# Kernel optimization log

Hardware: AMD Instinct MI355X
Metric: run time of the kernel (lower is better)

## Reference

```python
import jax, jax.numpy as jnp
import numpy as np

B, P, F_IN, F_OUT = 4, 256, 512, 512
TAU = 0.07
EPS = 1e-05


def setup_inputs() -> dict:
    key = jax.random.key(0)
    k1, k2, k3 = jax.random.split(key, 3)
    inputs = jax.random.normal(k1, (B, P, F_IN), dtype=jnp.float32)
    labels = jax.random.normal(k2, (B, P, F_IN), dtype=jnp.float32)
    # xavier_uniform for fc.weight (out, in)
    limit = float(np.sqrt(6.0 / (F_IN + F_OUT)))
    W = jax.random.uniform(k3, (F_OUT, F_IN), dtype=jnp.float32, minval=-limit, maxval=limit)
    b = jnp.zeros((F_OUT,), dtype=jnp.float32)
    return {"inputs": inputs, "labels": labels, "W": W, "b": b}


def reference(inputs, labels, W, b):
    Bz, Pn, _ = labels.shape
    # pairwise L1 distance between label vectors: (B, P, P)
    d = jnp.sum(jnp.abs(labels[:, None, :, :] - labels[:, :, None, :]), axis=-1)
    idx = (d == 0).astype(jnp.float32)
    dist = idx / jnp.sum(idx, axis=-1, keepdims=True)  # (B, P, P) target distribution
    # fc + L2 normalize (torch F.normalize: divide by max(norm, 1e-12))
    h = jnp.einsum("bpf,of->bpo", inputs, W) + b
    nrm = jnp.sqrt(jnp.sum(h * h, axis=-1, keepdims=True))
    x = h / jnp.maximum(nrm, 1e-12)
    scores = jnp.einsum("bpd,bqd->bpq", x, x) / TAU
    probs = jnp.clip(jax.nn.softmax(scores, axis=-1), EPS, 1.0 - EPS)
    # kl_div(log(probs), dist, reduction='batchmean'): sum(dist*(log(dist)-log(probs))) / (B*P)
    log_probs = jnp.log(probs)
    pointwise = jnp.where(dist > 0, dist * (jnp.log(jnp.where(dist > 0, dist, 1.0)) - log_probs), 0.0)
    loss = jnp.sum(pointwise) / (Bz * Pn)
    return loss
```

## Files before the change

kernel.cpp:

```cpp
#include <hip/hip_runtime.h>


#define INV_TAU (1.0f / 0.07f)
#define EPSC 1e-5f

constexpr int Bz = 4;
constexpr int Pn = 256;
constexpr int Fdim = 512;
constexpr int Mrows = Bz * Pn;
constexpr size_t HP_STRIDE = (size_t)Mrows * Fdim;
constexpr size_t SP_STRIDE = (size_t)Bz * Pn * Pn;

__device__ __forceinline__ float wave_sum(float v) {
  #pragma unroll
  for (int o = 32; o > 0; o >>= 1) v += __shfl_down(v, o, 64);
  return v;
}
__device__ __forceinline__ float wave_max(float v) {
  #pragma unroll
  for (int o = 32; o > 0; o >>= 1) v = fmaxf(v, __shfl_down(v, o, 64));
  return v;
}
__device__ __forceinline__ unsigned long long mix64(unsigned long long z) {
  z ^= z >> 33; z *= 0xff51afd7ed558ccdULL;
  z ^= z >> 33; z *= 0xc4ceb9fe1a85ec53ULL;
  z ^= z >> 33; return z;
}

__global__ __launch_bounds__(512) void fc_sig(const float* __restrict__ A,
                                              const float* __restrict__ W,
                                              const float* __restrict__ labels,
                                              float* __restrict__ hp,
                                              ulonglong2* __restrict__ sig,
                                              float* __restrict__ acc,
                                              unsigned int* __restrict__ done) {
  const int t = threadIdx.x;
  const int bid = blockIdx.x + 16 * (blockIdx.y + 8 * blockIdx.z);
  if (bid == 0 && t == 0) { acc[0] = 0.0f; done[0] = 0u; }

  {
    const int g = t >> 6, lane = t & 63;
    if (g < 4) {
      const int row = bid * 4 + g;
      const uint4* l4 = (const uint4*)(labels + (size_t)row * Fdim);
      unsigned long long h1 = 0, h2 = 0;
      #pragma unroll
      for (int c = lane; c < Fdim / 4; c += 64) {
        uint4 w = l4[c];
        unsigned long long w01 = ((unsigned long long)w.y << 32) | w.x;
        unsigned long long w23 = ((unsigned long long)w.w << 32) | w.z;
        unsigned long long idx = (unsigned long long)c;
        h1 ^= mix64(w01 + idx * 0x9E3779B97F4A7C15ULL + 0x0123456789ABCDEFULL);
        h1 ^= mix64(w23 + idx * 0xC2B2AE3D27D4EB4FULL + 1ULL);
        h2 ^= mix64(w01 ^ (idx * 0x165667B19E3779F9ULL + 7ULL));
        h2 ^= mix64(w23 ^ (idx * 0x27D4EB2F165667C5ULL + 13ULL));
      }
      #pragma unroll
      for (int o = 32; o > 0; o >>= 1) {
        h1 ^= __shfl_down(h1, o, 64);
        h2 ^= __shfl_down(h2, o, 64);
      }
      if (lane == 0) { sig[row].x = h1; sig[row].y = h2; }
    }
  }

  const int m0 = blockIdx.x * 64, n0 = blockIdx.y * 64;
  const int kbase = blockIdx.z * 256;
  float* C = hp + (size_t)blockIdx.z * HP_STRIDE;
  __shared__ float Ash[32][68];
  __shared__ float Bsh[32][68];
  const int tx = t & 15, ty = t >> 4;
  const int r0 = t >> 3, c0 = (t & 7) << 2;
  float acc2[2][4] = {};

  for (int kc = 0; kc < 256; kc += 32) {
    const float* Ap = A + (size_t)(m0 + r0) * Fdim + kbase + kc + c0;
    const float* Wp = W + (size_t)(n0 + r0) * Fdim + kbase + kc + c0;
    float4 a = *(const float4*)Ap;
    float4 b = *(const float4*)Wp;
    __syncthreads();
    Ash[c0+0][r0] = a.x; Ash[c0+1][r0] = a.y; Ash[c0+2][r0] = a.z; Ash[c0+3][r0] = a.w;
    Bsh[c0+0][r0] = b.x; Bsh[c0+1][r0] = b.y; Bsh[c0+2][r0] = b.z; Bsh[c0+3][r0] = b.w;
    __syncthreads();
    #pragma unroll 8
    for (int k = 0; k < 32; ++k) {
      float2 av = *(const float2*)&Ash[k][ty << 1];
      float4 bv = *(const float4*)&Bsh[k][tx << 2];
      acc2[0][0] = fmaf(av.x, bv.x, acc2[0][0]); acc2[0][1] = fmaf(av.x, bv.y, acc2[0][1]);
      acc2[0][2] = fmaf(av.x, bv.z, acc2[0][2]); acc2[0][3] = fmaf(av.x, bv.w, acc2[0][3]);
      acc2[1][0] = fmaf(av.y, bv.x, acc2[1][0]); acc2[1][1] = fmaf(av.y, bv.y, acc2[1][1]);
      acc2[1][2] = fmaf(av.y, bv.z, acc2[1][2]); acc2[1][3] = fmaf(av.y, bv.w, acc2[1][3]);
    }
  }
  #pragma unroll
  for (int i = 0; i < 2; ++i) {
    float4 o; o.x = acc2[i][0]; o.y = acc2[i][1]; o.z = acc2[i][2]; o.w = acc2[i][3];
    *(float4*)(C + (size_t)(m0 + (ty << 1) + i) * Fdim + n0 + (tx << 2)) = o;
  }
}

__global__ __launch_bounds__(512) void score_gemm(const float* __restrict__ hp,
                                                  const float* __restrict__ bias,
                                                  float* __restrict__ Sp) {
  const int b = blockIdx.z >> 2, kz = blockIdx.z & 3;
  const int kbase = kz * 128;
  const int m0 = blockIdx.x * 64, n0 = blockIdx.y * 64;
  const float* h0 = hp;
  const float* h1 = hp + HP_STRIDE;
  float* C = Sp + (size_t)kz * SP_STRIDE + (size_t)b * Pn * Pn;
  const size_t rb = (size_t)b * Pn;
  __shared__ float Ash[32][68];
  __shared__ float Bsh[32][68];
  const int t = threadIdx.x, tx = t & 15, ty = t >> 4;
  const int r0 = t >> 3, c0 = (t & 7) << 2;
  float acc2[2][4] = {};

  for (int kc = 0; kc < 128; kc += 32) {
    const int ko = kbase + kc + c0;
    float4 bi = *(const float4*)(bias + ko);
    size_t aoff = (rb + m0 + r0) * Fdim + ko;
    size_t boff = (rb + n0 + r0) * Fdim + ko;
    float4 al = *(const float4*)(h0 + aoff);
    float4 ah = *(const float4*)(h1 + aoff);
    float4 bl = *(const float4*)(h0 + boff);
    float4 bh = *(const float4*)(h1 + boff);
    float4 a, b;
    a.x = al.x + ah.x + bi.x; a.y = al.y + ah.y + bi.y;
    a.z = al.z + ah.z + bi.z; a.w = al.w + ah.w + bi.w;
    b.x = bl.x + bh.x + bi.x; b.y = bl.y + bh.y + bi.y;
    b.z = bl.z + bh.z + bi.z; b.w = bl.w + bh.w + bi.w;
    __syncthreads();
    Ash[c0+0][r0] = a.x; Ash[c0+1][r0] = a.y; Ash[c0+2][r0] = a.z; Ash[c0+3][r0] = a.w;
    Bsh[c0+0][r0] = b.x; Bsh[c0+1][r0] = b.y; Bsh[c0+2][r0] = b.z; Bsh[c0+3][r0] = b.w;
    __syncthreads();
    #pragma unroll 8
    for (int k = 0; k < 32; ++k) {
      float2 av = *(const float2*)&Ash[k][ty << 1];
      float4 bv = *(const float4*)&Bsh[k][tx << 2];
      acc2[0][0] = fmaf(av.x, bv.x, acc2[0][0]); acc2[0][1] = fmaf(av.x, bv.y, acc2[0][1]);
      acc2[0][2] = fmaf(av.x, bv.z, acc2[0][2]); acc2[0][3] = fmaf(av.x, bv.w, acc2[0][3]);
      acc2[1][0] = fmaf(av.y, bv.x, acc2[1][0]); acc2[1][1] = fmaf(av.y, bv.y, acc2[1][1]);
      acc2[1][2] = fmaf(av.y, bv.z, acc2[1][2]); acc2[1][3] = fmaf(av.y, bv.w, acc2[1][3]);
    }
  }
  #pragma unroll
  for (int i = 0; i < 2; ++i) {
    float4 o; o.x = acc2[i][0]; o.y = acc2[i][1]; o.z = acc2[i][2]; o.w = acc2[i][3];
    *(float4*)(C + (size_t)(m0 + (ty << 1) + i) * Pn + n0 + (tx << 2)) = o;
  }
}

__global__ __launch_bounds__(256) void loss_kernel(const float* __restrict__ Sp,
                                                   const ulonglong2* __restrict__ sig,
                                                   const float* __restrict__ labels,
                                                   float* __restrict__ acc,
                                                   unsigned int* __restrict__ done,
                                                   float* __restrict__ out) {
  const int bx = blockIdx.x;
  const int b = bx >> 6, p0 = (bx & 63) * 4;
  const int q = threadIdx.x;
  __shared__ float invn[256];
  __shared__ float red[12];
  const float* S0 = Sp + (size_t)b * Pn * Pn;
  const float* S1 = S0 + SP_STRIDE;
  const float* S2 = S0 + 2 * SP_STRIDE;
  const float* S3 = S0 + 3 * SP_STRIDE;

  {
    const int d = q * 257;
    float Sqq = S0[d] + S1[d] + S2[d] + S3[d];
    invn[q] = 1.0f / fmaxf(sqrtf(Sqq), 1e-12f);
  }
  const ulonglong2 sq = sig[(b << 8) + q];
  __syncthreads();

  const int w = q >> 6;
  float lane_contrib = 0.0f;

  #pragma unroll
  for (int i = 0; i < 4; ++i) {
    const int p = p0 + i;
    const int ro = p << 8;
    float Spq = S0[ro + q] + S1[ro + q] + S2[ro + q] + S3[ro + q];
    float s = Spq * invn[p] * invn[q] * INV_TAU;

    ulonglong2 sp = sig[(b << 8) + p];
    bool eq;
    if (q == p) eq = true;
    else if (sp.x == sq.x && sp.y == sq.y) {
      bool v = true;
      const float* lp = labels + (size_t)((b << 8) + p) * Fdim;
      const float* lq = labels + (size_t)((b << 8) + q) * Fdim;
      for (int j = 0; j < Fdim; ++j) v = v && (lp[j] == lq[j]);
      eq = v;
    } else eq = false;

    float m = wave_max(s);
    if ((q & 63) == 0) red[w] = m;
    __syncthreads();
    m = fmaxf(fmaxf(red[0], red[1]), fmaxf(red[2], red[3]));

    float e = expf(s - m);
    float zc = wave_sum(e);
    float cc = wave_sum(eq ? 1.0f : 0.0f);
    if ((q & 63) == 0) { red[4 + w] = zc; red[8 + w] = cc; }
    __syncthreads();
    float z = red[4] + red[5] + red[6] + red[7];
    float n = red[8] + red[9] + red[10] + red[11];

    float prob = fminf(fmaxf(e / z, EPSC), 1.0f - EPSC);
    if (eq) lane_contrib += (-logf(n) - logf(prob)) / n;
    __syncthreads();
  }

  float c = wave_sum(lane_contrib);
  if ((q & 63) == 0) red[w] = c;
  __syncthreads();
  if (q == 0) {
    atomicAdd(acc, red[0] + red[1] + red[2] + red[3]);
    __threadfence();
    unsigned int v = atomicAdd(done, 1u);
    if (v == 255u) {
      float tot = atomicAdd(acc, 0.0f);
      out[0] = tot * (1.0f / (float)(Bz * Pn));
    }
  }
}

extern "C" void kernel_launch(void* const* d_in, const int* in_sizes, int n_in,
                              void* d_out, int out_size, void* d_ws, size_t ws_size,
                              hipStream_t stream) {
  const float* inputs = (const float*)d_in[0];
  const float* labels = (const float*)d_in[1];
  const float* W      = (const float*)d_in[2];
  const float* bias   = (const float*)d_in[3];
  float* out = (float*)d_out;

  char* ws = (char*)d_ws;
  float* acc         = (float*)ws;
  unsigned int* done = (unsigned int*)(ws + 4);
  float* hp = (float*)(ws + 256);
  float* Sp = (float*)(ws + 256 + 2 * HP_STRIDE * 4);
  ulonglong2* sig = (ulonglong2*)(ws + 256 + 2 * HP_STRIDE * 4 + 4 * SP_STRIDE * 4);

  fc_sig<<<dim3(16, 8, 2), 512, 0, stream>>>(inputs, W, labels, hp, sig, acc, done);
  score_gemm<<<dim3(4, 4, 16), 512, 0, stream>>>(hp, bias, Sp);
  loss_kernel<<<256, 256, 0, stream>>>(Sp, sig, labels, acc, done, out);
}
```

Measured before the change: 99.07 us.

## Double-buffer GEMM tiles, 4x4 microtiles, fold bias, restructure loss softmax per wave

Both GEMM kernels now run 256 threads, each computing a 4x4 register microtile, and prefetch the next K-slice into registers while computing on a double-buffered shared-memory tile. This drops one barrier per iteration and overlaps global loads with FMAs. The bias is added once in the first FC split instead of on every score-GEMM load, and the score GEMM writes the diagonal norms to a small buffer. The loss kernel assigns one row per wave with four columns per lane, removing block-level barriers from the softmax reductions. The trade-offs are fewer threads per block and higher register pressure.

```diff
diff --git a/kernel.cpp b/kernel.cpp
--- a/kernel.cpp
+++ b/kernel.cpp
@@ -13,12 +13,12 @@
 
 __device__ __forceinline__ float wave_sum(float v) {
   #pragma unroll
-  for (int o = 32; o > 0; o >>= 1) v += __shfl_down(v, o, 64);
+  for (int o = 32; o > 0; o >>= 1) v += __shfl_xor(v, o, 64);
   return v;
 }
 __device__ __forceinline__ float wave_max(float v) {
   #pragma unroll
-  for (int o = 32; o > 0; o >>= 1) v = fmaxf(v, __shfl_down(v, o, 64));
+  for (int o = 32; o > 0; o >>= 1) v = fmaxf(v, __shfl_xor(v, o, 64));
   return v;
 }
 __device__ __forceinline__ unsigned long long mix64(unsigned long long z) {
@@ -27,8 +27,9 @@
   z ^= z >> 33; return z;
 }
 
-__global__ __launch_bounds__(512) void fc_sig(const float* __restrict__ A,
+__global__ __launch_bounds__(256) void fc_sig(const float* __restrict__ A,
                                               const float* __restrict__ W,
+                                              const float* __restrict__ bias,
                                               const float* __restrict__ labels,
                                               float* __restrict__ hp,
                                               ulonglong2* __restrict__ sig,
@@ -40,68 +41,100 @@
 
   {
     const int g = t >> 6, lane = t & 63;
-    if (g < 4) {
-      const int row = bid * 4 + g;
-      const uint4* l4 = (const uint4*)(labels + (size_t)row * Fdim);
-      unsigned long long h1 = 0, h2 = 0;
-      #pragma unroll
-      for (int c = lane; c < Fdim / 4; c += 64) {
-        uint4 w = l4[c];
-        unsigned long long w01 = ((unsigned long long)w.y << 32) | w.x;
-        unsigned long long w23 = ((unsigned long long)w.w << 32) | w.z;
-        unsigned long long idx = (unsigned long long)c;
-        h1 ^= mix64(w01 + idx * 0x9E3779B97F4A7C15ULL + 0x0123456789ABCDEFULL);
-        h1 ^= mix64(w23 + idx * 0xC2B2AE3D27D4EB4FULL + 1ULL);
-        h2 ^= mix64(w01 ^ (idx * 0x165667B19E3779F9ULL + 7ULL));
-        h2 ^= mix64(w23 ^ (idx * 0x27D4EB2F165667C5ULL + 13ULL));
-      }
-      #pragma unroll
-      for (int o = 32; o > 0; o >>= 1) {
-        h1 ^= __shfl_down(h1, o, 64);
-        h2 ^= __shfl_down(h2, o, 64);
-      }
-      if (lane == 0) { sig[row].x = h1; sig[row].y = h2; }
-    }
+    const int row = bid * 4 + g;
+    const uint4* l4 = (const uint4*)(labels + (size_t)row * Fdim);
+    unsigned long long h1 = 0, h2 = 0;
+    #pragma unroll
+    for (int c = lane; c < Fdim / 4; c += 64) {
+      uint4 wv = l4[c];
+      unsigned long long w01 = ((unsigned long long)wv.y << 32) | wv.x;
+      unsigned long long w23 = ((unsigned long long)wv.w << 32) | wv.z;
+      unsigned long long idx = (unsigned long long)c;
+      h1 ^= mix64(w01 + idx * 0x9E3779B97F4A7C15ULL + 0x0123456789ABCDEFULL);
+      h1 ^= mix64(w23 + idx * 0xC2B2AE3D27D4EB4FULL + 1ULL);
+      h2 ^= mix64(w01 ^ (idx * 0x165667B19E3779F9ULL + 7ULL));
+      h2 ^= mix64(w23 ^ (idx * 0x27D4EB2F165667C5ULL + 13ULL));
+    }
+    #pragma unroll
+    for (int o = 32; o > 0; o >>= 1) {
+      h1 ^= __shfl_down(h1, o, 64);
+      h2 ^= __shfl_down(h2, o, 64);
+    }
+    if (lane == 0) { sig[row].x = h1; sig[row].y = h2; }
   }
 
   const int m0 = blockIdx.x * 64, n0 = blockIdx.y * 64;
   const int kbase = blockIdx.z * 256;
   float* C = hp + (size_t)blockIdx.z * HP_STRIDE;
-  __shared__ float Ash[32][68];
-  __shared__ float Bsh[32][68];
+  __shared__ float Ash[2][32][68];
+  __shared__ float Bsh[2][32][68];
   const int tx = t & 15, ty = t >> 4;
-  const int r0 = t >> 3, c0 = (t & 7) << 2;
-  float acc2[2][4] = {};
-
+  const int sr = t >> 3, sc = (t & 7) << 2;
+
+  const float* Abase = A + (size_t)(m0 + sr) * Fdim + kbase + sc;
+  const float* Wbase = W + (size_t)(n0 + sr) * Fdim + kbase + sc;
+  float4 ra0, ra1, rb0, rb1;
+
+  auto store_tile = [&](int buf) {
+    Ash[buf][sc+0][sr] = ra0.x; Ash[buf][sc+1][sr] = ra0.y;
+    Ash[buf][sc+2][sr] = ra0.z; Ash[buf][sc+3][sr] = ra0.w;
+    Ash[buf][sc+0][sr+32] = ra1.x; Ash[buf][sc+1][sr+32] = ra1.y;
+    Ash[buf][sc+2][sr+32] = ra1.z; Ash[buf][sc+3][sr+32] = ra1.w;
+    Bsh[buf][sc+0][sr] = rb0.x; Bsh[buf][sc+1][sr] = rb0.y;
+    Bsh[buf][sc+2][sr] = rb0.z; Bsh[buf][sc+3][sr] = rb0.w;
+    Bsh[buf][sc+0][sr+32] = rb1.x; Bsh[buf][sc+1][sr+32] = rb1.y;
+    Bsh[buf][sc+2][sr+32] = rb1.z; Bsh[buf][sc+3][sr+32] = rb1.w;
+  };
+
+  ra0 = *(const float4*)(Abase);
+  ra1 = *(const float4*)(Abase + 32 * Fdim);
+  rb0 = *(const float4*)(Wbase);
+  rb1 = *(const float4*)(Wbase + 32 * Fdim);
+  store_tile(0);
+  __syncthreads();
+
+  float acc4[4][4] = {};
+
+  #pragma unroll
   for (int kc = 0; kc < 256; kc += 32) {
-    const float* Ap = A + (size_t)(m0 + r0) * Fdim + kbase + kc + c0;
-    const float* Wp = W + (size_t)(n0 + r0) * Fdim + kbase + kc + c0;
-    float4 a = *(const float4*)Ap;
-    float4 b = *(const float4*)Wp;
-    __syncthreads();
-    Ash[c0+0][r0] = a.x; Ash[c0+1][r0] = a.y; Ash[c0+2][r0] = a.z; Ash[c0+3][r0] = a.w;
-    Bsh[c0+0][r0] = b.x; Bsh[c0+1][r0] = b.y; Bsh[c0+2][r0] = b.z; Bsh[c0+3][r0] = b.w;
-    __syncthreads();
+    const int cur = (kc >> 5) & 1;
+    if (kc + 32 < 256) {
+      ra0 = *(const float4*)(Abase + kc + 32);
+      ra1 = *(const float4*)(Abase + kc + 32 + 32 * Fdim);
+      rb0 = *(const float4*)(Wbase + kc + 32);
+      rb1 = *(const float4*)(Wbase + kc + 32 + 32 * Fdim);
+    }
     #pragma unroll 8
     for (int k = 0; k < 32; ++k) {
-      float2 av = *(const float2*)&Ash[k][ty << 1];
-      float4 bv = *(const float4*)&Bsh[k][tx << 2];
-      acc2[0][0] = fmaf(av.x, bv.x, acc2[0][0]); acc2[0][1] = fmaf(av.x, bv.y, acc2[0][1]);
-      acc2[0][2] = fmaf(av.x, bv.z, acc2[0][2]); acc2[0][3] = fmaf(av.x, bv.w, acc2[0][3]);
-      acc2[1][0] = fmaf(av.y, bv.x, acc2[1][0]); acc2[1][1] = fmaf(av.y, bv.y, acc2[1][1]);
-      acc2[1][2] = fmaf(av.y, bv.z, acc2[1][2]); acc2[1][3] = fmaf(av.y, bv.w, acc2[1][3]);
-    }
-  }
-  #pragma unroll
-  for (int i = 0; i < 2; ++i) {
-    float4 o; o.x = acc2[i][0]; o.y = acc2[i][1]; o.z = acc2[i][2]; o.w = acc2[i][3];
-    *(float4*)(C + (size_t)(m0 + (ty << 1) + i) * Fdim + n0 + (tx << 2)) = o;
-  }
-}
-
-__global__ __launch_bounds__(512) void score_gemm(const float* __restrict__ hp,
-                                                  const float* __restrict__ bias,
-                                                  float* __restrict__ Sp) {
+      float4 av = *(const float4*)&Ash[cur][k][ty << 2];
+      float4 bv = *(const float4*)&Bsh[cur][k][tx << 2];
+      acc4[0][0] = fmaf(av.x, bv.x, acc4[0][0]); acc4[0][1] = fmaf(av.x, bv.y, acc4[0][1]);
+      acc4[0][2] = fmaf(av.x, bv.z, acc4[0][2]); acc4[0][3] = fmaf(av.x, bv.w, acc4[0][3]);
+      acc4[1][0] = fmaf(av.y, bv.x, acc4[1][0]); acc4[1][1] = fmaf(av.y, bv.y, acc4[1][1]);
+      acc4[1][2] = fmaf(av.y, bv.z, acc4[1][2]); acc4[1][3] = fmaf(av.y, bv.w, acc4[1][3]);
+      acc4[2][0] = fmaf(av.z, bv.x, acc4[2][0]); acc4[2][1] = fmaf(av.z, bv.y, acc4[2][1]);
+      acc4[2][2] = fmaf(av.z, bv.z, acc4[2][2]); acc4[2][3] = fmaf(av.z, bv.w, acc4[2][3]);
+      acc4[3][0] = fmaf(av.w, bv.x, acc4[3][0]); acc4[3][1] = fmaf(av.w, bv.y, acc4[3][1]);
+      acc4[3][2] = fmaf(av.w, bv.z, acc4[3][2]); acc4[3][3] = fmaf(av.w, bv.w, acc4[3][3]);
+    }
+    if (kc + 32 < 256) store_tile(cur ^ 1);
+    __syncthreads();
+  }
+
+  float4 bi = make_float4(0.0f, 0.0f, 0.0f, 0.0f);
+  if (blockIdx.z == 0) bi = *(const float4*)(bias + n0 + (tx << 2));
+  #pragma unroll
+  for (int i = 0; i < 4; ++i) {
+    float4 o;
+    o.x = acc4[i][0] + bi.x; o.y = acc4[i][1] + bi.y;
+    o.z = acc4[i][2] + bi.z; o.w = acc4[i][3] + bi.w;
+    *(float4*)(C + (size_t)(m0 + (ty << 2) + i) * Fdim + n0 + (tx << 2)) = o;
+  }
+}
+
+__global__ __launch_bounds__(256) void score_gemm(const float* __restrict__ hp,
+                                                  float* __restrict__ Sp,
+                                                  float* __restrict__ dn) {
   const int b = blockIdx.z >> 2, kz = blockIdx.z & 3;
   const int kbase = kz * 128;
   const int m0 = blockIdx.x * 64, n0 = blockIdx.y * 64;
@@ -109,112 +142,155 @@
   const float* h1 = hp + HP_STRIDE;
   float* C = Sp + (size_t)kz * SP_STRIDE + (size_t)b * Pn * Pn;
   const size_t rb = (size_t)b * Pn;
-  __shared__ float Ash[32][68];
-  __shared__ float Bsh[32][68];
+  __shared__ float Ash[2][32][68];
+  __shared__ float Bsh[2][32][68];
   const int t = threadIdx.x, tx = t & 15, ty = t >> 4;
-  const int r0 = t >> 3, c0 = (t & 7) << 2;
-  float acc2[2][4] = {};
-
+  const int sr = t >> 3, sc = (t & 7) << 2;
+  const size_t aoff = (rb + m0 + sr) * Fdim + kbase + sc;
+  const size_t boff = (rb + n0 + sr) * Fdim + kbase + sc;
+
+  float4 la0, ha0, la1, ha1, lb0, hb0, lb1, hb1;
+
+  auto load_tile = [&](int kc) {
+    la0 = *(const float4*)(h0 + aoff + kc);
+    ha0 = *(const float4*)(h1 + aoff + kc);
+    la1 = *(const float4*)(h0 + aoff + kc + 32 * Fdim);
+    ha1 = *(const float4*)(h1 + aoff + kc + 32 * Fdim);
+    lb0 = *(const float4*)(h0 + boff + kc);
+    hb0 = *(const float4*)(h1 + boff + kc);
+    lb1 = *(const float4*)(h0 + boff + kc + 32 * Fdim);
+    hb1 = *(const float4*)(h1 + boff + kc + 32 * Fdim);
+  };
+  auto store_tile = [&](int buf) {
+    float4 a0, a1, b0v, b1v;
+    a0.x = la0.x + ha0.x; a0.y = la0.y + ha0.y; a0.z = la0.z + ha0.z; a0.w = la0.w + ha0.w;
+    a1.x = la1.x + ha1.x; a1.y = la1.y + ha1.y; a1.z = la1.z + ha1.z; a1.w = la1.w + ha1.w;
+    b0v.x = lb0.x + hb0.x; b0v.y = lb0.y + hb0.y; b0v.z = lb0.z + hb0.z; b0v.w = lb0.w + hb0.w;
+    b1v.x = lb1.x + hb1.x; b1v.y = lb1.y + hb1.y; b1v.z = lb1.z + hb1.z; b1v.w = lb1.w + hb1.w;
+    Ash[buf][sc+0][sr] = a0.x; Ash[buf][sc+1][sr] = a0.y;
+    Ash[buf][sc+2][sr] = a0.z; Ash[buf][sc+3][sr] = a0.w;
+    Ash[buf][sc+0][sr+32] = a1.x; Ash[buf][sc+1][sr+32] = a1.y;
+    Ash[buf][sc+2][sr+32] = a1.z; Ash[buf][sc+3][sr+32] = a1.w;
+    Bsh[buf][sc+0][sr] = b0v.x; Bsh[buf][sc+1][sr] = b0v.y;
+    Bsh[buf][sc+2][sr] = b0v.z; Bsh[buf][sc+3][sr] = b0v.w;
+    Bsh[buf][sc+0][sr+32] = b1v.x; Bsh[buf][sc+1][sr+32] = b1v.y;
+    Bsh[buf][sc+2][sr+32] = b1v.z; Bsh[buf][sc+3][sr+32] = b1v.w;
+  };
+
+  load_tile(0);
+  store_tile(0);
+  __syncthreads();
+
+  float acc4[4][4] = {};
+
+  #pragma unroll
   for (int kc = 0; kc < 128; kc += 32) {
-    const int ko = kbase + kc + c0;
-    float4 bi = *(const float4*)(bias + ko);
-    size_t aoff = (rb + m0 + r0) * Fdim + ko;
-    size_t boff = (rb + n0 + r0) * Fdim + ko;
-    float4 al = *(const float4*)(h0 + aoff);
-    float4 ah = *(const float4*)(h1 + aoff);
-    float4 bl = *(const float4*)(h0 + boff);
-    float4 bh = *(const float4*)(h1 + boff);
-    float4 a, b;
-    a.x = al.x + ah.x + bi.x; a.y = al.y + ah.y + bi.y;
-    a.z = al.z + ah.z + bi.z; a.w = al.w + ah.w + bi.w;
-    b.x = bl.x + bh.x + bi.x; b.y = bl.y + bh.y + bi.y;
-    b.z = bl.z + bh.z + bi.z; b.w = bl.w + bh.w + bi.w;
-    __syncthreads();
-    Ash[c0+0][r0] = a.x; Ash[c0+1][r0] = a.y; Ash[c0+2][r0] = a.z; Ash[c0+3][r0] = a.w;
-    Bsh[c0+0][r0] = b.x; Bsh[c0+1][r0] = b.y; Bsh[c0+2][r0] = b.z; Bsh[c0+3][r0] = b.w;
-    __syncthreads();
+    const int cur = (kc >> 5) & 1;
+    if (kc + 32 < 128) load_tile(kc + 32);
     #pragma unroll 8
     for (int k = 0; k < 32; ++k) {
-      float2 av = *(const float2*)&Ash[k][ty << 1];
-      float4 bv = *(const float4*)&Bsh[k][tx << 2];
-      acc2[0][0] = fmaf(av.x, bv.x, acc2[0][0]); acc2[0][1] = fmaf(av.x, bv.y, acc2[0][1]);
-      acc2[0][2] = fmaf(av.x, bv.z, acc2[0][2]); acc2[0][3] = fmaf(av.x, bv.w, acc2[0][3]);
-      acc2[1][0] = fmaf(av.y, bv.x, acc2[1][0]); acc2[1][1] = fmaf(av.y, bv.y, acc2[1][1]);
-      acc2[1][2] = fmaf(av.y, bv.z, acc2[1][2]); acc2[1][3] = fmaf(av.y, bv.w, acc2[1][3]);
-    }
-  }
-  #pragma unroll
-  for (int i = 0; i < 2; ++i) {
-    float4 o; o.x = acc2[i][0]; o.y = acc2[i][1]; o.z = acc2[i][2]; o.w = acc2[i][3];
-    *(float4*)(C + (size_t)(m0 + (ty << 1) + i) * Pn + n0 + (tx << 2)) = o;
+      float4 av = *(const float4*)&Ash[cur][k][ty << 2];
+      float4 bv = *(const float4*)&Bsh[cur][k][tx << 2];
+      acc4[0][0] = fmaf(av.x, bv.x, acc4[0][0]); acc4[0][1] = fmaf(av.x, bv.y, acc4[0][1]);
+      acc4[0][2] = fmaf(av.x, bv.z, acc4[0][2]); acc4[0][3] = fmaf(av.x, bv.w, acc4[0][3]);
+      acc4[1][0] = fmaf(av.y, bv.x, acc4[1][0]); acc4[1][1] = fmaf(av.y, bv.y, acc4[1][1]);
+      acc4[1][2] = fmaf(av.y, bv.z, acc4[1][2]); acc4[1][3] = fmaf(av.y, bv.w, acc4[1][3]);
+      acc4[2][0] = fmaf(av.z, bv.x, acc4[2][0]); acc4[2][1] = fmaf(av.z, bv.y, acc4[2][1]);
+      acc4[2][2] = fmaf(av.z, bv.z, acc4[2][2]); acc4[2][3] = fmaf(av.z, bv.w, acc4[2][3]);
+      acc4[3][0] = fmaf(av.w, bv.x, acc4[3][0]); acc4[3][1] = fmaf(av.w, bv.y, acc4[3][1]);
+      acc4[3][2] = fmaf(av.w, bv.z, acc4[3][2]); acc4[3][3] = fmaf(av.w, bv.w, acc4[3][3]);
+    }
+    if (kc + 32 < 128) store_tile(cur ^ 1);
+    __syncthreads();
+  }
+
+  #pragma unroll
+  for (int i = 0; i < 4; ++i) {
+    float4 o; o.x = acc4[i][0]; o.y = acc4[i][1]; o.z = acc4[i][2]; o.w = acc4[i][3];
+    *(float4*)(C + (size_t)(m0 + (ty << 2) + i) * Pn + n0 + (tx << 2)) = o;
+  }
+  if (m0 == n0 && tx == ty) {
+    #pragma unroll
+    for (int i = 0; i < 4; ++i)
+      dn[(size_t)kz * Mrows + rb + m0 + (ty << 2) + i] = acc4[i][i];
   }
 }
 
 __global__ __launch_bounds__(256) void loss_kernel(const float* __restrict__ Sp,
                                                    const ulonglong2* __restrict__ sig,
                                                    const float* __restrict__ labels,
+                                                   const float* __restrict__ dn,
                                                    float* __restrict__ acc,
                                                    unsigned int* __restrict__ done,
                                                    float* __restrict__ out) {
   const int bx = blockIdx.x;
   const int b = bx >> 6, p0 = (bx & 63) * 4;
   const int q = threadIdx.x;
+  const int w = q >> 6, lane = q & 63;
   __shared__ float invn[256];
-  __shared__ float red[12];
+  __shared__ float red[4];
   const float* S0 = Sp + (size_t)b * Pn * Pn;
   const float* S1 = S0 + SP_STRIDE;
   const float* S2 = S0 + 2 * SP_STRIDE;
   const float* S3 = S0 + 3 * SP_STRIDE;
 
   {
-    const int d = q * 257;
-    float Sqq = S0[d] + S1[d] + S2[d] + S3[d];
-    invn[q] = 1.0f / fmaxf(sqrtf(Sqq), 1e-12f);
-  }
-  const ulonglong2 sq = sig[(b << 8) + q];
+    const int iq = (b << 8) + q;
+    float d = dn[iq] + dn[Mrows + iq] + dn[2 * Mrows + iq] + dn[3 * Mrows + iq];
+    invn[q] = 1.0f / fmaxf(sqrtf(d), 1e-12f);
+  }
   __syncthreads();
 
-  const int w = q >> 6;
-  float lane_contrib = 0.0f;
-
-  #pragma unroll
-  for (int i = 0; i < 4; ++i) {
-    const int p = p0 + i;
-    const int ro = p << 8;
-    float Spq = S0[ro + q] + S1[ro + q] + S2[ro + q] + S3[ro + q];
-    float s = Spq * invn[p] * invn[q] * INV_TAU;
-
-    ulonglong2 sp = sig[(b << 8) + p];
+  const int p = p0 + w;
+  const int ro = p << 8;
+  const ulonglong2 sp = sig[(b << 8) + p];
+  const float ip = invn[p];
+
+  float s[4];
+  unsigned eqm = 0;
+  #pragma unroll
+  for (int c = 0; c < 4; ++c) {
+    const int qq = (c << 6) + lane;
+    float Sv = S0[ro + qq] + S1[ro + qq] + S2[ro + qq] + S3[ro + qq];
+    s[c] = Sv * ip * invn[qq] * INV_TAU;
     bool eq;
-    if (q == p) eq = true;
-    else if (sp.x == sq.x && sp.y == sq.y) {
-      bool v = true;
-      const float* lp = labels + (size_t)((b << 8) + p) * Fdim;
-      const float* lq = labels + (size_t)((b << 8) + q) * Fdim;
-      for (int j = 0; j < Fdim; ++j) v = v && (lp[j] == lq[j]);
-      eq = v;
-    } else eq = false;
-
-    float m = wave_max(s);
-    if ((q & 63) == 0) red[w] = m;
-    __syncthreads();
-    m = fmaxf(fmaxf(red[0], red[1]), fmaxf(red[2], red[3]));
-
-    float e = expf(s - m);
-    float zc = wave_sum(e);
-    float cc = wave_sum(eq ? 1.0f : 0.0f);
-    if ((q & 63) == 0) { red[4 + w] = zc; red[8 + w] = cc; }
-    __syncthreads();
-    float z = red[4] + red[5] + red[6] + red[7];
-    float n = red[8] + red[9] + red[10] + red[11];
-
-    float prob = fminf(fmaxf(e / z, EPSC), 1.0f - EPSC);
-    if (eq) lane_contrib += (-logf(n) - logf(prob)) / n;
-    __syncthreads();
-  }
-
-  float c = wave_sum(lane_contrib);
-  if ((q & 63) == 0) red[w] = c;
+    if (qq == p) eq = true;
+    else {
+      ulonglong2 sq = sig[(b << 8) + qq];
+      if (sq.x == sp.x && sq.y == sp.y) {
+        bool v = true;
+        const float* lp = labels + (size_t)((b << 8) + p) * Fdim;
+        const float* lq = labels + (size_t)((b << 8) + qq) * Fdim;
+        for (int j = 0; j < Fdim; ++j) v = v && (lp[j] == lq[j]);
+        eq = v;
+      } else eq = false;
+    }
+    if (eq) eqm |= (1u << c);
+  }
+
+  float m = fmaxf(fmaxf(s[0], s[1]), fmaxf(s[2], s[3]));
+  m = wave_max(m);
+
+  float e[4], z = 0.0f, n = 0.0f;
+  #pragma unroll
+  for (int c = 0; c < 4; ++c) {
+    e[c] = expf(s[c] - m);
+    z += e[c];
+    n += ((eqm >> c) & 1u) ? 1.0f : 0.0f;
+  }
+  z = wave_sum(z);
+  n = wave_sum(n);
+
+  float contrib = 0.0f;
+  #pragma unroll
+  for (int c = 0; c < 4; ++c) {
+    if ((eqm >> c) & 1u) {
+      float prob = fminf(fmaxf(e[c] / z, EPSC), 1.0f - EPSC);
+      contrib += (-logf(n) - logf(prob)) / n;
+    }
+  }
+  contrib = wave_sum(contrib);
+  if (lane == 0) red[w] = contrib;
   __syncthreads();
   if (q == 0) {
     atomicAdd(acc, red[0] + red[1] + red[2] + red[3]);
@@ -242,8 +318,10 @@
   float* hp = (float*)(ws + 256);
   float* Sp = (float*)(ws + 256 + 2 * HP_STRIDE * 4);
   ulonglong2* sig = (ulonglong2*)(ws + 256 + 2 * HP_STRIDE * 4 + 4 * SP_STRIDE * 4);
-
-  fc_sig<<<dim3(16, 8, 2), 512, 0, stream>>>(inputs, W, labels, hp, sig, acc, done);
-  score_gemm<<<dim3(4, 4, 16), 512, 0, stream>>>(hp, bias, Sp);
-  loss_kernel<<<256, 256, 0, stream>>>(Sp, sig, labels, acc, done, out);
-}
+  float* dn = (float*)(ws + 256 + 2 * HP_STRIDE * 4 + 4 * SP_STRIDE * 4
+                       + (size_t)Mrows * sizeof(ulonglong2));
+
+  fc_sig<<<dim3(16, 8, 2), 256, 0, stream>>>(inputs, W, bias, labels, hp, sig, acc, done);
+  score_gemm<<<dim3(4, 4, 16), 256, 0, stream>>>(hp, Sp, dn);
+  loss_kernel<<<256, 256, 0, stream>>>(Sp, sig, labels, dn, acc, done, out);
+}
```

New measurement: 95.52 us, median of 2. 1.04x faster.
